# Kernel tuning notes

Hardware: AMD Instinct MI355X
Metric: run time of the kernel (lower is better)

Reference implementation:

```python
import jax, jax.numpy as jnp
import numpy as np

B = 4          # graphs
N = 8192       # coarse nodes (2048/graph)
M = 65536      # fine (skip) nodes (16384/graph)
E = 131072     # edges (32768/graph)
T = 16         # global tokens per graph
F_IN = 16      # dim of x and x_skip (concat -> in_channels = 32)
HID, OUT = 32, 16
ED, GD, EMB, H = 3, 1024, 64, 4
K = 3


def _make_pe(t, d):
    # PositionalEncoding buffer (sin/cos), deterministic constant
    position = np.arange(t, dtype=np.float32)[:, None]
    div = np.exp(np.arange(0, d, 2, dtype=np.float32) * (-np.log(10000.0) / d))
    pe = np.zeros((t, d), dtype=np.float32)
    pe[:, 0::2] = np.sin(position * div)
    pe[:, 1::2] = np.cos(position * div)
    return jnp.asarray(pe)


def setup_inputs():
    key = jax.random.key(0)
    ks = jax.random.split(key, 30)
    n, m, e = N // B, M // B, E // B
    inp = {}
    inp['x'] = jax.random.normal(ks[0], (N, F_IN), jnp.float32)
    inp['pos'] = jax.random.normal(ks[1], (N, 3), jnp.float32)
    inp['batch'] = jnp.repeat(jnp.arange(B), n)
    inp['x_skip'] = jax.random.normal(ks[2], (M, F_IN), jnp.float32)
    inp['pos_skip'] = jax.random.normal(ks[3], (M, 3), jnp.float32)
    inp['batch_skip'] = jnp.repeat(jnp.arange(B), m)
    off = jnp.repeat(jnp.arange(B) * m, e)
    inp['edge_index'] = jax.random.randint(ks[4], (2, E), 0, m) + off[None, :]
    inp['global_token'] = jax.random.normal(ks[5], (B * T, GD), jnp.float32)
    def lin(k, o, i, s):
        return jax.random.normal(k, (o, i), jnp.float32) * s
    inp['Wq_w'] = lin(ks[6], EMB, ED, 0.3); inp['Wq_b'] = jnp.zeros((EMB,), jnp.float32)
    inp['Wk_w'] = lin(ks[7], EMB, GD, 0.03); inp['Wk_b'] = jnp.zeros((EMB,), jnp.float32)
    inp['Wv_w'] = lin(ks[8], EMB, GD, 0.03); inp['Wv_b'] = jnp.zeros((EMB,), jnp.float32)
    inp['in_proj_w'] = lin(ks[9], 3 * EMB, EMB, 0.125); inp['in_proj_b'] = jnp.zeros((3 * EMB,), jnp.float32)
    inp['out_w'] = lin(ks[10], EMB, EMB, 0.125); inp['out_b'] = jnp.zeros((EMB,), jnp.float32)
    dims = [(2 * F_IN, HID), (HID, HID), (HID, OUT)]
    for i, (ci, co) in enumerate(dims):
        inp[f'nn_w{i}'] = lin(ks[11 + 3 * i], ci * co, ED + EMB, 0.05)
        inp[f'nn_b{i}'] = jnp.zeros((ci * co,), jnp.float32)
        inp[f'root{i}'] = jax.random.normal(ks[12 + 3 * i], (ci, co), jnp.float32) * (1.0 / np.sqrt(ci))
        inp[f'bias{i}'] = jnp.zeros((co,), jnp.float32)
    return inp


def reference(x, pos, batch, x_skip, pos_skip, batch_skip, edge_index, global_token,
              Wq_w, Wq_b, Wk_w, Wk_b, Wv_w, Wv_b, in_proj_w, in_proj_b, out_w, out_b,
              nn_w0, nn_b0, root0, bias0, nn_w1, nn_b1, root1, bias1, nn_w2, nn_b2, root2, bias2):
    # ---- knn_interpolate (k=3, inverse squared-distance weighting) ----
    # graphs are equal-sized by construction so per-graph knn == batched knn
    pos_b = pos.reshape(B, -1, 3)
    posk_b = pos_skip.reshape(B, -1, 3)
    d2 = ((posk_b ** 2).sum(-1)[:, :, None] + (pos_b ** 2).sum(-1)[:, None, :]
          - 2.0 * jnp.einsum('bmc,bnc->bmn', posk_b, pos_b))  # [B,m,n]
    neg, idx = jax.lax.top_k(-d2, K)                           # [B,m,K]
    w = 1.0 / jnp.maximum(-neg, 1e-16)
    x_b = x.reshape(B, -1, x.shape[-1])
    feats = jnp.take_along_axis(x_b[:, None, :, :], idx[:, :, :, None], axis=2)  # [B,m,K,F]
    xf = ((w[..., None] * feats).sum(2) / w.sum(2)[..., None]).reshape(M, -1)

    src, dst = edge_index[0], edge_index[1]
    pseudo = pos_skip[dst] - pos_skip[src]                     # patch_size is None
    edge_pos = (0.5 * (pos_skip[dst] + pos_skip[src])).reshape(B, -1, 3)
    gt = global_token.reshape(B, -1, global_token.shape[-1])
    pe = _make_pe(gt.shape[1], EMB)
    Q = edge_pos @ Wq_w.T + Wq_b                               # [B,Eb,EMB]
    Kt = gt @ Wk_w.T + Wk_b + pe                               # dropout in eval = identity
    Vt = gt @ Wv_w.T + Wv_b + pe
    # ---- MultiheadAttention (batch_first) ----
    wq, wk, wv = jnp.split(in_proj_w, 3, axis=0)
    bq, bk, bv = jnp.split(in_proj_b, 3, axis=0)
    hd = EMB // H
    def heads(t, w_, b_):
        t = t @ w_.T + b_
        return t.reshape(t.shape[0], t.shape[1], H, hd).transpose(0, 2, 1, 3)
    q, k_, v = heads(Q, wq, bq), heads(Kt, wk, bk), heads(Vt, wv, bv)
    att = jax.nn.softmax(jnp.einsum('bhqd,bhkd->bhqk', q, k_) / np.sqrt(hd).astype(np.float32), axis=-1)
    o = jnp.einsum('bhqk,bhkd->bhqd', att, v).transpose(0, 2, 1, 3).reshape(B, -1, EMB)
    o = o @ out_w.T + out_b
    pseudo = jnp.concatenate([pseudo, o.reshape(-1, EMB)], axis=-1)  # [E, 3+64]

    # ---- NNConv stack (gather -> edge MLP -> per-edge matmul -> scatter mean) ----
    h = jnp.concatenate([xf, x_skip], axis=1)                  # [M, 32]
    ones = jnp.ones((E,), jnp.float32)
    cnt = jnp.maximum(jax.ops.segment_sum(ones, dst, num_segments=M), 1.0)[:, None]
    for nw, nb, rt, bs in ((nn_w0, nn_b0, root0, bias0),
                           (nn_w1, nn_b1, root1, bias1),
                           (nn_w2, nn_b2, root2, bias2)):
        ci, co = rt.shape
        we = jax.nn.relu(pseudo @ nw.T + nb).reshape(E, ci, co)  # MLP (BN at default eval stats ~ identity)
        msg = jnp.einsum('ei,eio->eo', h[src], we)               # [E, co]
        aggr = jax.ops.segment_sum(msg, dst, num_segments=M) / cnt
        h = jax.nn.relu(aggr + h @ rt + bs)                      # drop_act=False -> relu every layer
    return h, pos_skip, batch_skip
```

## Files before the change

kernel.cpp:

```cpp
#include <hip/hip_runtime.h>
#include <math.h>

#define NB    4
#define NN    8192
#define MM    65536
#define EE    131072
#define NPG   2048

typedef short short8 __attribute__((ext_vector_type(8)));
typedef float f32x4  __attribute__((ext_vector_type(4)));

static __device__ inline unsigned short f2b(float f) {
    unsigned u = __float_as_uint(f);
    u += 0x7fffu + ((u >> 16) & 1u);
    return (unsigned short)(u >> 16);
}
static __device__ inline unsigned f2b_pack(float a, float b) {
    unsigned x = __float_as_uint(a); x += 0x7fffu + ((x >> 16) & 1u);
    unsigned y = __float_as_uint(b); y += 0x7fffu + ((y >> 16) & 1u);
    return (x >> 16) | (y & 0xffff0000u);
}
static __device__ inline short8 bc8(uint4 v) {
    union { uint4 u; short8 s; } c; c.u = v; return c.s;
}

__global__ __launch_bounds__(256)
void k_knn(const float* __restrict__ pos, const float* __restrict__ pos_skip,
           const float* __restrict__ x, const float* __restrict__ x_skip,
           const int* __restrict__ batch_skip,
           float* __restrict__ h0, float* __restrict__ out_pos,
           float* __restrict__ out_batch)
{
    __shared__ float4 cp[1024];
    __shared__ float  pk[8][32][3];
    __shared__ float  wFin[32][3];
    __shared__ int    iFin[32][3];

    int tid = threadIdx.x;
    int g = blockIdx.x >> 9;
    int cbase = g * NPG;
    int node = tid & 31;
    int slice = tid >> 5;
    int fbase = blockIdx.x * 32;
    int f = fbase + node;
    float fx = pos_skip[f * 3 + 0], fy = pos_skip[f * 3 + 1], fz = pos_skip[f * 3 + 2];

    float k0 = 3.4028235e38f, k1 = 3.4028235e38f, k2 = 3.4028235e38f;
#pragma unroll
    for (int p = 0; p < 2; ++p) {
        if (p) __syncthreads();
        for (int c = tid; c < 1024; c += 256) {
            int cc = cbase + p * 1024 + c;
            float px = pos[cc * 3 + 0];
            float py = pos[cc * 3 + 1];
            float pz = pos[cc * 3 + 2];
            cp[c] = make_float4(-2.f * px, -2.f * py, -2.f * pz,
                                px * px + py * py + pz * pz);
        }
        __syncthreads();
        const float4* cps = cp + slice * 128;
        unsigned ibase = (unsigned)(p * 128);
#pragma unroll 8
        for (int l = 0; l < 128; ++l) {
            float4 cc = cps[l];
            float d = fmaf(cc.x, fx, cc.w);
            d = fmaf(cc.y, fy, d);
            d = fmaf(cc.z, fz, d);
            float key = __uint_as_float((__float_as_uint(d) & 0xFFFFFF00u)
                                        | (ibase + (unsigned)l));
            float t = fmaxf(k1, key);
            k2 = fminf(k2, t);
            k1 = __builtin_amdgcn_fmed3f(k0, k1, key);
            k0 = fminf(k0, key);
        }
    }
    pk[slice][node][0] = k0; pk[slice][node][1] = k1; pk[slice][node][2] = k2;
    __syncthreads();

    if (tid < 32) {
        int n = tid;
        int fn = fbase + n;
        float gx = pos_skip[fn * 3 + 0], gy = pos_skip[fn * 3 + 1], gz = pos_skip[fn * 3 + 2];
        float gq = gx * gx + gy * gy + gz * gz;
        unsigned long long m0 = ~0ull, m1 = ~0ull, m2 = ~0ull;
#pragma unroll
        for (int s = 0; s < 8; ++s)
#pragma unroll
            for (int r = 0; r < 3; ++r) {
                unsigned key = __float_as_uint(pk[s][n][r]);
                unsigned pj = key & 255u;
                int c = cbase + (int)((pj >> 7) * 1024u + (unsigned)s * 128u + (pj & 127u));
                float px = pos[c * 3 + 0];
                float py = pos[c * 3 + 1];
                float pz = pos[c * 3 + 2];
                float d = gq + (px * px + py * py + pz * pz);
                d = fmaf(-2.f * px, gx, d);
                d = fmaf(-2.f * py, gy, d);
                d = fmaf(-2.f * pz, gz, d);
                d = fmaxf(d, 0.f);
                unsigned long long kk = ((unsigned long long)__float_as_uint(d) << 32) | (unsigned)c;
                unsigned long long t1 = m0 > kk ? m0 : kk; m0 = m0 < kk ? m0 : kk;
                unsigned long long t2 = m1 > t1 ? m1 : t1; m1 = m1 < t1 ? m1 : t1;
                m2 = m2 < t2 ? m2 : t2;
            }
        float d0 = __uint_as_float((unsigned)(m0 >> 32));
        float d1 = __uint_as_float((unsigned)(m1 >> 32));
        float d2 = __uint_as_float((unsigned)(m2 >> 32));
        float w0 = 1.f / fmaxf(d0, 1e-16f);
        float w1 = 1.f / fmaxf(d1, 1e-16f);
        float w2 = 1.f / fmaxf(d2, 1e-16f);
        float inv = 1.f / (w0 + w1 + w2);
        wFin[n][0] = w0 * inv; wFin[n][1] = w1 * inv; wFin[n][2] = w2 * inv;
        iFin[n][0] = (int)(m0 & 0xffffffffull);
        iFin[n][1] = (int)(m1 & 0xffffffffull);
        iFin[n][2] = (int)(m2 & 0xffffffffull);
        out_pos[fn * 3 + 0] = gx; out_pos[fn * 3 + 1] = gy; out_pos[fn * 3 + 2] = gz;
        out_batch[fn] = (float)batch_skip[fn];
    }
    __syncthreads();

    int n2 = tid >> 3, part = tid & 7;
    int f2 = fbase + n2;
    float4* h04 = (float4*)(h0 + (size_t)f2 * 32);
    if (part < 4) {
        const float4* x4 = (const float4*)x;
        float w0 = wFin[n2][0], w1 = wFin[n2][1], w2 = wFin[n2][2];
        int a0 = iFin[n2][0] * 4, a1 = iFin[n2][1] * 4, a2 = iFin[n2][2] * 4;
        float4 v0 = x4[a0 + part], v1 = x4[a1 + part], v2 = x4[a2 + part];
        float4 r;
        r.x = w0 * v0.x + w1 * v1.x + w2 * v2.x;
        r.y = w0 * v0.y + w1 * v1.y + w2 * v2.y;
        r.z = w0 * v0.z + w1 * v1.z + w2 * v2.z;
        r.w = w0 * v0.w + w1 * v1.w + w2 * v2.w;
        h04[part] = r;
    } else {
        const float4* xs4 = (const float4*)x_skip;
        h04[part] = xs4[f2 * 4 + (part - 4)];
    }
}

__global__ __launch_bounds__(128)
void k_tokens1(const float* __restrict__ gt,
               const float* __restrict__ Wk_w, const float* __restrict__ Wk_b,
               const float* __restrict__ Wv_w, const float* __restrict__ Wv_b,
               float* __restrict__ KtVt)
{
    int b = blockIdx.x >> 4;
    int t = blockIdx.x & 15;
    int which = threadIdx.x >> 6;
    int d = threadIdx.x & 63;
    const float* W = which ? Wv_w : Wk_w;
    const float* bias = which ? Wv_b : Wk_b;
    const float4* row = (const float4*)(gt + (size_t)(b * 16 + t) * 1024);
    const float4* wr = (const float4*)(W + (size_t)d * 1024);
    float acc = 0.f;
    for (int c = 0; c < 256; ++c) {
        float4 a = row[c], w = wr[c];
        acc += a.x * w.x; acc += a.y * w.y; acc += a.z * w.z; acc += a.w * w.w;
    }
    int i2 = d >> 1;
    float dv = expf((float)(2 * i2) * (-0.14391156831212787f));
    float ang = (float)t * dv;
    float pe = (d & 1) ? cosf(ang) : sinf(ang);
    KtVt[((size_t)(b * 2 + which) * 16 + t) * 64 + d] = acc + bias[d] + pe;
}

__global__ __launch_bounds__(256)
void k_tokens2(const float* __restrict__ KtVt,
               const float* __restrict__ in_proj_w, const float* __restrict__ in_proj_b,
               const float* __restrict__ out_w,
               const float* __restrict__ Wq_w, const float* __restrict__ Wq_b,
               float* __restrict__ Mfold, uint4* __restrict__ v2fG)
{
    int b = blockIdx.x;
    int tid = threadIdx.x;
    __shared__ float KtL[1024], VtL[1024], vv[1024], kproj[1024];
    __shared__ float v2L[4096];
    __shared__ float qWs[192], qbs[64];
    for (int idx = tid; idx < 1024; idx += 256) {
        KtL[idx] = KtVt[(size_t)(b * 2 + 0) * 1024 + idx];
        VtL[idx] = KtVt[(size_t)(b * 2 + 1) * 1024 + idx];
    }
    __syncthreads();
    for (int idx = tid; idx < 2048; idx += 256) {
        int which = idx >> 10; int td = idx & 1023; int t = td >> 6; int j = td & 63;
        int r = (which ? 128 : 64) + j;
        const float* w = in_proj_w + (size_t)r * 64;
        const float* src = which ? VtL : KtL;
        float acc = in_proj_b[r];
#pragma unroll 8
        for (int dd = 0; dd < 64; ++dd) acc += src[t * 64 + dd] * w[dd];
        if (which) vv[t * 64 + j] = acc;
        else kproj[t * 64 + j] = acc;
    }
    for (int idx = tid; idx < 192; idx += 256) {
        int c = idx >> 6; int j = idx & 63;
        float acc = 0.f;
        for (int dd = 0; dd < 64; ++dd) acc += in_proj_w[(size_t)j * 64 + dd] * Wq_w[dd * 3 + c];
        qWs[c * 64 + j] = acc;
    }
    for (int j = tid; j < 64; j += 256) {
        float acc = in_proj_b[j];
        for (int dd = 0; dd < 64; ++dd) acc += in_proj_w[(size_t)j * 64 + dd] * Wq_b[dd];
        qbs[j] = acc;
    }
    __syncthreads();
    for (int idx = tid; idx < 4096; idx += 256) {
        int jo = idx & 63; int th2 = idx >> 6; int h = th2 & 3; int t = th2 >> 2;
        float acc = 0.f;
#pragma unroll
        for (int dd = 0; dd < 16; ++dd)
            acc += vv[t * 64 + h * 16 + dd] * out_w[(size_t)jo * 64 + h * 16 + dd];
        v2L[(t * 4 + h) * 64 + jo] = acc;
    }
    {
        int th = tid >> 2, c = tid & 3;
        int t = th >> 2, h = th & 3;
        float acc = 0.f;
#pragma unroll
        for (int dd = h * 16; dd < h * 16 + 16; ++dd) {
            float w = (c == 0) ? qWs[dd] : (c == 1) ? qWs[64 + dd]
                    : (c == 2) ? qWs[128 + dd] : qbs[dd];
            acc += w * kproj[t * 64 + dd];
        }
        Mfold[((size_t)b * 64 + th) * 4 + c] = 0.25f * acc;
    }
    __syncthreads();
    for (int it = tid; it < 512; it += 256) {
        int lane = it & 63, fi = it >> 6;
        int mi = fi >> 1, step = fi & 1;
        int outd = mi * 16 + (lane & 15);
        int th0 = step * 32 + (lane >> 4) * 8;
        uint4 v;
        v.x = f2b_pack(v2L[(th0 + 0) * 64 + outd], v2L[(th0 + 1) * 64 + outd]);
        v.y = f2b_pack(v2L[(th0 + 2) * 64 + outd], v2L[(th0 + 3) * 64 + outd]);
        v.z = f2b_pack(v2L[(th0 + 4) * 64 + outd], v2L[(th0 + 5) * 64 + outd]);
        v.w = f2b_pack(v2L[(th0 + 6) * 64 + outd], v2L[(th0 + 7) * 64 + outd]);
        v2fG[((size_t)b * 8 + fi) * 64 + lane] = v;
    }
}

__global__ __launch_bounds__(256)
void k_edge_attn(const float* __restrict__ ps, const int* __restrict__ ei,
                 const float* __restrict__ Mfold, const uint4* __restrict__ v2f,
                 const float* __restrict__ ob,
                 unsigned short* __restrict__ Pf, float* __restrict__ cnt)
{
    __shared__ unsigned attL[4 * 64 * 34];
    int tid = threadIdx.x;
    int wave = tid >> 6, lane = tid & 63, q = lane >> 4, c15 = lane & 15;
    int g = blockIdx.x >> 7;
    int e = blockIdx.x * 256 + tid;
    int s = ei[e], d = ei[EE + e];
    atomicAdd(&cnt[d], 1.f);
    float sx = ps[s * 3], sy = ps[s * 3 + 1], sz = ps[s * 3 + 2];
    float dx = ps[d * 3], dy = ps[d * 3 + 1], dz = ps[d * 3 + 2];
    float px = dx - sx, py = dy - sy, pz = dz - sz;
    float ex = 0.5f * (dx + sx), ey = 0.5f * (dy + sy), ez = 0.5f * (dz + sz);

    const float4* Mg = (const float4*)Mfold + (size_t)g * 64;
    float sc[64];
#pragma unroll
    for (int th = 0; th < 64; ++th) {
        float4 m = Mg[th];
        sc[th] = ex * m.x + ey * m.y + ez * m.z + m.w;
    }
#pragma unroll
    for (int h = 0; h < 4; ++h) {
        float mx = sc[h];
#pragma unroll
        for (int t = 1; t < 16; ++t) mx = fmaxf(mx, sc[t * 4 + h]);
        float ssum = 0.f;
#pragma unroll
        for (int t = 0; t < 16; ++t) {
            float eo = expf(sc[t * 4 + h] - mx);
            sc[t * 4 + h] = eo; ssum += eo;
        }
        float inv = 1.f / ssum;
#pragma unroll
        for (int t = 0; t < 16; ++t) sc[t * 4 + h] *= inv;
    }
    unsigned* slab = attL + wave * 64 * 34;
#pragma unroll
    for (int k = 0; k < 16; ++k) {
        uint2 v;
        v.x = f2b_pack(sc[4 * k + 0], sc[4 * k + 1]);
        v.y = f2b_pack(sc[4 * k + 2], sc[4 * k + 3]);
        *(uint2*)&slab[lane * 34 + 2 * k] = v;
    }
    __syncthreads();

    uint4 v2a[4][2];
#pragma unroll
    for (int mi = 0; mi < 4; ++mi)
#pragma unroll
        for (int st = 0; st < 2; ++st)
            v2a[mi][st] = v2f[((size_t)g * 8 + mi * 2 + st) * 64 + lane];

    f32x4 acc[4][4];
#pragma unroll
    for (int mi = 0; mi < 4; ++mi)
#pragma unroll
        for (int nt = 0; nt < 4; ++nt) acc[mi][nt] = (f32x4){0.f, 0.f, 0.f, 0.f};

#pragma unroll
    for (int nt = 0; nt < 4; ++nt) {
        const unsigned* rb = &slab[(nt * 16 + c15) * 34];
        uint4 b0 = *(const uint4*)&rb[q * 4];
        uint4 b1 = *(const uint4*)&rb[16 + q * 4];
#pragma unroll
        for (int mi = 0; mi < 4; ++mi) {
            acc[mi][nt] = __builtin_amdgcn_mfma_f32_16x16x32_bf16(bc8(v2a[mi][0]), bc8(b0), acc[mi][nt], 0, 0, 0);
            acc[mi][nt] = __builtin_amdgcn_mfma_f32_16x16x32_bf16(bc8(v2a[mi][1]), bc8(b1), acc[mi][nt], 0, 0, 0);
        }
    }
    __syncthreads();

    float4 obv[4];
#pragma unroll
    for (int mi = 0; mi < 4; ++mi) obv[mi] = *(const float4*)(ob + mi * 16 + q * 4);
#pragma unroll
    for (int mi = 0; mi < 4; ++mi)
#pragma unroll
        for (int nt = 0; nt < 4; ++nt) {
            f32x4 a = acc[mi][nt];
            uint2 v;
            v.x = f2b_pack(a[0] + obv[mi].x, a[1] + obv[mi].y);
            v.y = f2b_pack(a[2] + obv[mi].z, a[3] + obv[mi].w);
            *(uint2*)&slab[(nt * 16 + c15) * 34 + mi * 8 + q * 2] = v;
        }
    __syncthreads();

    uint4* Pf4 = (uint4*)Pf;
#pragma unroll
    for (int et = 0; et < 4; ++et) {
        int etg = blockIdx.x * 16 + wave * 4 + et;
#pragma unroll
        for (int st = 0; st < 2; ++st) {
            uint4 w = *(const uint4*)&slab[(et * 16 + c15) * 34 + st * 16 + q * 4];
            Pf4[((size_t)etg * 3 + st) * 64 + lane] = w;
        }
    }
    int et2 = e >> 4, eL = e & 15;
    size_t tb = ((size_t)(et2 * 3 + 2) * 64 + 0 * 16 + eL) * 8;
    uint2 t0; t0.x = f2b_pack(px, py); t0.y = f2b_pack(pz, 1.0f);
    *(uint2*)(Pf + tb) = t0;
    uint2 z2; z2.x = 0u; z2.y = 0u;
    *(uint2*)(Pf + tb + 4) = z2;
#pragma unroll
    for (int quad = 1; quad < 4; ++quad) {
        size_t zb = ((size_t)(et2 * 3 + 2) * 64 + quad * 16 + eL) * 8;
        uint4 z4; z4.x = 0u; z4.y = 0u; z4.z = 0u; z4.w = 0u;
        *(uint4*)(Pf + zb) = z4;
    }
}

static __device__ inline void repack_one(const float* __restrict__ nw,
                                         const float* __restrict__ nb,
                                         unsigned short* __restrict__ Wf, int idx)
{
    int jj = idx & 7;
    int lane = (idx >> 3) & 63;
    int rest = idx >> 9;
    int s = rest % 3;
    int jt = rest / 3;
    int j = jt * 16 + (lane & 15);
    int k = s * 32 + (lane >> 4) * 8 + jj;
    float v;
    if (k < 64)       v = nw[(size_t)j * 67 + 3 + k];
    else if (k < 67)  v = nw[(size_t)j * 67 + (k - 64)];
    else if (k == 67) v = nb[j];
    else              v = 0.f;
    Wf[idx] = f2b(v);
}

__global__ __launch_bounds__(256)
void k_repackAll(const float* __restrict__ nw0, const float* __restrict__ nb0,
                 const float* __restrict__ nw1, const float* __restrict__ nb1,
                 const float* __restrict__ nw2, const float* __restrict__ nb2,
                 unsigned short* __restrict__ Wf0, unsigned short* __restrict__ Wf1,
                 unsigned short* __restrict__ Wf2)
{
    int idx = blockIdx.x * 256 + threadIdx.x;
    if (idx < 98304)        repack_one(nw0, nb0, Wf0, idx);
    else if (idx < 196608)  repack_one(nw1, nb1, Wf1, idx - 98304);
    else                    repack_one(nw2, nb2, Wf2, idx - 196608);
}

template<int CO>
__global__ __launch_bounds__(256, 4)
void k_conv_mfma(const uint4* __restrict__ Pf, const float* __restrict__ hin,
                 const int* __restrict__ ei, const uint4* __restrict__ Wf,
                 float* __restrict__ aggr)
{
    __shared__ float hL[128 * 36];
    __shared__ int sL[128];
    __shared__ int dL[128];
    constexpr int REDSZ = (CO == 16) ? 2 * 64 * 17 : 4;
    __shared__ float red[REDSZ];

    int tid = threadIdx.x;
    int e0 = blockIdx.x * 128;
    if (tid < 128) sL[tid] = ei[e0 + tid];
    else           dL[tid - 128] = ei[EE + e0 + (tid - 128)];
    __syncthreads();
    for (int idx = tid; idx < 1024; idx += 256) {
        int row = idx >> 3, c = idx & 7;
        const float4* hr = (const float4*)(hin + (size_t)sL[row] * 32);
        *(float4*)&hL[row * 36 + c * 4] = hr[c];
    }
    __syncthreads();

    int wave = tid >> 6, lane = tid & 63, quad = lane >> 4, col = lane & 15;
    int group = wave >> 1, half = wave & 1;

    uint4 a[4][3];
    int et0 = blockIdx.x * 8 + group * 4;
#pragma unroll
    for (int st = 0; st < 4; ++st)
#pragma unroll
        for (int s = 0; s < 3; ++s)
            a[st][s] = Pf[((size_t)(et0 + st) * 3 + s) * 64 + lane];

    float msg[4][4];
#pragma unroll
    for (int st = 0; st < 4; ++st)
#pragma unroll
        for (int r = 0; r < 4; ++r) msg[st][r] = 0.f;

    int ibase = (CO == 32) ? 0 : half * 16;
    constexpr int NI2 = (CO == 32) ? 16 : 8;

    for (int i2 = 0; i2 < NI2; ++i2) {
        float2 hv2[4][4];
#pragma unroll
        for (int st = 0; st < 4; ++st)
#pragma unroll
            for (int r = 0; r < 4; ++r)
                hv2[st][r] = *(const float2*)&hL[(group * 64 + st * 16 + quad * 4 + r) * 36
                                                 + ibase + i2 * 2];
#pragma unroll
        for (int ii = 0; ii < 2; ++ii) {
            int i = ibase + i2 * 2 + ii;
            int jt = (CO == 32) ? (i * 2 + half) : i;
            uint4 b0 = Wf[((size_t)jt * 3 + 0) * 64 + lane];
            uint4 b1 = Wf[((size_t)jt * 3 + 1) * 64 + lane];
            uint4 b2 = Wf[((size_t)jt * 3 + 2) * 64 + lane];
#pragma unroll
            for (int st = 0; st < 4; ++st) {
                f32x4 c = {0.f, 0.f, 0.f, 0.f};
                c = __builtin_amdgcn_mfma_f32_16x16x32_bf16(bc8(a[st][0]), bc8(b0), c, 0, 0, 0);
                c = __builtin_amdgcn_mfma_f32_16x16x32_bf16(bc8(a[st][1]), bc8(b1), c, 0, 0, 0);
                c = __builtin_amdgcn_mfma_f32_16x16x32_bf16(bc8(a[st][2]), bc8(b2), c, 0, 0, 0);
#pragma unroll
                for (int r = 0; r < 4; ++r) {
                    float hv = ii ? hv2[st][r].y : hv2[st][r].x;
                    msg[st][r] += hv * fmaxf(c[r], 0.f);
                }
            }
        }
    }

    if (CO == 32) {
#pragma unroll
        for (int st = 0; st < 4; ++st)
#pragma unroll
            for (int r = 0; r < 4; ++r) {
                int dv = dL[group * 64 + st * 16 + quad * 4 + r];
                atomicAdd(&aggr[(size_t)dv * 32 + half * 16 + col], msg[st][r]);
            }
    } else {
        if (half == 1) {
#pragma unroll
            for (int st = 0; st < 4; ++st)
#pragma unroll
                for (int r = 0; r < 4; ++r)
                    red[group * 64 * 17 + lane * 17 + st * 4 + r] = msg[st][r];
        }
        __syncthreads();
        if (half == 0) {
#pragma unroll
            for (int st = 0; st < 4; ++st)
#pragma unroll
                for (int r = 0; r < 4; ++r) {
                    float m = msg[st][r] + red[group * 64 * 17 + lane * 17 + st * 4 + r];
                    int dv = dL[group * 64 + st * 16 + quad * 4 + r];
                    atomicAdd(&aggr[(size_t)dv * 16 + col], m);
                }
        }
    }
}

template<int CO>
__global__ __launch_bounds__(256)
void k_update(float* __restrict__ aggr, const float* __restrict__ cnt,
              const float* __restrict__ hin, const float* __restrict__ root,
              const float* __restrict__ bias, float* __restrict__ hout)
{
    __shared__ float rL[32 * CO];
    __shared__ float bL[CO];
    int tid = threadIdx.x;
    for (int idx = tid; idx < 32 * CO; idx += 256) rL[idx] = root[idx];
    if (tid < CO) bL[tid] = bias[tid];
    __syncthreads();
    int gid = blockIdx.x * 256 + tid;
    int v = gid / CO;
    int o = gid % CO;
    float acc = aggr[gid] / fmaxf(cnt[v], 1.f) + bL[o];
    aggr[gid] = 0.f;
    const float* hr = hin + (size_t)v * 32;
#pragma unroll
    for (int i = 0; i < 32; ++i) acc += hr[i] * rL[i * CO + o];
    hout[gid] = fmaxf(acc, 0.f);
}

extern "C" void kernel_launch(void* const* d_in, const int* in_sizes, int n_in,
                              void* d_out, int out_size, void* d_ws, size_t ws_size,
                              hipStream_t stream)
{
    const float* x          = (const float*)d_in[0];
    const float* pos        = (const float*)d_in[1];
    const float* x_skip     = (const float*)d_in[3];
    const float* pos_skip   = (const float*)d_in[4];
    const int*   batch_skip = (const int*)  d_in[5];
    const int*   ei         = (const int*)  d_in[6];
    const float* gt         = (const float*)d_in[7];
    const float* Wq_w       = (const float*)d_in[8];
    const float* Wq_b       = (const float*)d_in[9];
    const float* Wk_w       = (const float*)d_in[10];
    const float* Wk_b       = (const float*)d_in[11];
    const float* Wv_w       = (const float*)d_in[12];
    const float* Wv_b       = (const float*)d_in[13];
    const float* in_proj_w  = (const float*)d_in[14];
    const float* in_proj_b  = (const float*)d_in[15];
    const float* out_w      = (const float*)d_in[16];
    const float* out_b      = (const float*)d_in[17];
    const float* nn_w0 = (const float*)d_in[18]; const float* nn_b0 = (const float*)d_in[19];
    const float* root0 = (const float*)d_in[20]; const float* bias0 = (const float*)d_in[21];
    const float* nn_w1 = (const float*)d_in[22]; const float* nn_b1 = (const float*)d_in[23];
    const float* root1 = (const float*)d_in[24]; const float* bias1 = (const float*)d_in[25];
    const float* nn_w2 = (const float*)d_in[26]; const float* nn_b2 = (const float*)d_in[27];
    const float* root2 = (const float*)d_in[28]; const float* bias2 = (const float*)d_in[29];

    char* wsb = (char*)d_ws;
    size_t off = 0;
    auto carve = [&](size_t bytes) { char* p = wsb + off; off += (bytes + 255) & ~(size_t)255; return p; };
    float* aggr = (float*)carve((size_t)MM * 32 * 4);
    float* cnt  = (float*)carve((size_t)MM * 4);
    float* hA   = (float*)carve((size_t)MM * 32 * 4);
    float* hB   = (float*)carve((size_t)MM * 32 * 4);
    unsigned short* Pf  = (unsigned short*)carve((size_t)EE * 96 * 2);
    unsigned short* Wf0 = (unsigned short*)carve((size_t)1024 * 96 * 2);
    unsigned short* Wf1 = (unsigned short*)carve((size_t)1024 * 96 * 2);
    unsigned short* Wf2 = (unsigned short*)carve((size_t)512 * 96 * 2);
    float* Mfold = (float*)carve((size_t)NB * 64 * 4 * 4);
    uint4* v2f   = (uint4*)carve((size_t)NB * 8 * 64 * 16);
    float* KtVt  = (float*)carve((size_t)NB * 2 * 16 * 64 * 4);

    float* h_final   = (float*)d_out;
    float* out_pos   = (float*)d_out + (size_t)MM * 16;
    float* out_batch = (float*)d_out + (size_t)MM * 19;

    hipMemsetAsync(aggr, 0, ((size_t)MM * 32 + MM) * sizeof(float), stream);

    k_tokens1<<<64, 128, 0, stream>>>(gt, Wk_w, Wk_b, Wv_w, Wv_b, KtVt);
    k_tokens2<<<NB, 256, 0, stream>>>(KtVt, in_proj_w, in_proj_b, out_w, Wq_w, Wq_b,
                                      Mfold, v2f);
    k_knn<<<MM / 32, 256, 0, stream>>>(pos, pos_skip, x, x_skip, batch_skip,
                                       hA, out_pos, out_batch);
    k_edge_attn<<<EE / 256, 256, 0, stream>>>(pos_skip, ei, Mfold, v2f, out_b,
                                              Pf, cnt);
    k_repackAll<<<960, 256, 0, stream>>>(nn_w0, nn_b0, nn_w1, nn_b1, nn_w2, nn_b2,
                                         Wf0, Wf1, Wf2);

    k_conv_mfma<32><<<EE / 128, 256, 0, stream>>>((const uint4*)Pf, hA, ei, (const uint4*)Wf0, aggr);
    k_update<32><<<(MM * 32) / 256, 256, 0, stream>>>(aggr, cnt, hA, root0, bias0, hB);
    k_conv_mfma<32><<<EE / 128, 256, 0, stream>>>((const uint4*)Pf, hB, ei, (const uint4*)Wf1, aggr);
    k_update<32><<<(MM * 32) / 256, 256, 0, stream>>>(aggr, cnt, hB, root1, bias1, hA);
    k_conv_mfma<16><<<EE / 128, 256, 0, stream>>>((const uint4*)Pf, hA, ei, (const uint4*)Wf2, aggr);
    k_update<16><<<(MM * 16) / 256, 256, 0, stream>>>(aggr, cnt, hA, root2, bias2, h_final);
}
```

Measured before the change: 366.2 us.

## Register-block kNN so each thread scans candidates for four fine nodes

The kNN kernel now handles 64 fine nodes per block instead of 32. Each thread keeps top-3 state for four fine nodes and scans a 64-candidate slice, so every LDS candidate load is reused across four distance evaluations. Coarse positions are staged into shared memory half as often per fine node, and the block count is halved. The cost is more registers per thread, a 16-way merge in the final stage instead of 8-way, and a longer serial refine step running on only 64 threads.

```diff
diff --git a/kernel.cpp b/kernel.cpp
--- a/kernel.cpp
+++ b/kernel.cpp
@@ -32,20 +32,28 @@
            float* __restrict__ out_batch)
 {
     __shared__ float4 cp[1024];
-    __shared__ float  pk[8][32][3];
-    __shared__ float  wFin[32][3];
-    __shared__ int    iFin[32][3];
+    __shared__ float  pk[16][64][3];
+    __shared__ float  wFin[64][3];
+    __shared__ int    iFin[64][3];
 
     int tid = threadIdx.x;
-    int g = blockIdx.x >> 9;
+    int g = blockIdx.x >> 8;
     int cbase = g * NPG;
-    int node = tid & 31;
-    int slice = tid >> 5;
-    int fbase = blockIdx.x * 32;
-    int f = fbase + node;
-    float fx = pos_skip[f * 3 + 0], fy = pos_skip[f * 3 + 1], fz = pos_skip[f * 3 + 2];
-
-    float k0 = 3.4028235e38f, k1 = 3.4028235e38f, k2 = 3.4028235e38f;
+    int slice = tid & 15;
+    int grp = tid >> 4;
+    int fbase = blockIdx.x * 64;
+
+    float fx[4], fy[4], fz[4];
+    float k0[4], k1[4], k2[4];
+#pragma unroll
+    for (int j = 0; j < 4; ++j) {
+        int f = fbase + grp * 4 + j;
+        fx[j] = pos_skip[f * 3 + 0];
+        fy[j] = pos_skip[f * 3 + 1];
+        fz[j] = pos_skip[f * 3 + 2];
+        k0[j] = 3.4028235e38f; k1[j] = 3.4028235e38f; k2[j] = 3.4028235e38f;
+    }
+
 #pragma unroll
     for (int p = 0; p < 2; ++p) {
         if (p) __syncthreads();
@@ -58,38 +66,45 @@
                                 px * px + py * py + pz * pz);
         }
         __syncthreads();
-        const float4* cps = cp + slice * 128;
-        unsigned ibase = (unsigned)(p * 128);
-#pragma unroll 8
-        for (int l = 0; l < 128; ++l) {
+        const float4* cps = cp + slice * 64;
+        unsigned ibase = (unsigned)(p * 64);
+#pragma unroll 4
+        for (int l = 0; l < 64; ++l) {
             float4 cc = cps[l];
-            float d = fmaf(cc.x, fx, cc.w);
-            d = fmaf(cc.y, fy, d);
-            d = fmaf(cc.z, fz, d);
-            float key = __uint_as_float((__float_as_uint(d) & 0xFFFFFF00u)
-                                        | (ibase + (unsigned)l));
-            float t = fmaxf(k1, key);
-            k2 = fminf(k2, t);
-            k1 = __builtin_amdgcn_fmed3f(k0, k1, key);
-            k0 = fminf(k0, key);
-        }
-    }
-    pk[slice][node][0] = k0; pk[slice][node][1] = k1; pk[slice][node][2] = k2;
-    __syncthreads();
-
-    if (tid < 32) {
+            unsigned idx = ibase + (unsigned)l;
+#pragma unroll
+            for (int j = 0; j < 4; ++j) {
+                float d = fmaf(cc.x, fx[j], cc.w);
+                d = fmaf(cc.y, fy[j], d);
+                d = fmaf(cc.z, fz[j], d);
+                float key = __uint_as_float((__float_as_uint(d) & 0xFFFFFF00u) | idx);
+                float t = fmaxf(k1[j], key);
+                k2[j] = fminf(k2[j], t);
+                k1[j] = __builtin_amdgcn_fmed3f(k0[j], k1[j], key);
+                k0[j] = fminf(k0[j], key);
+            }
+        }
+    }
+#pragma unroll
+    for (int j = 0; j < 4; ++j) {
+        int n = grp * 4 + j;
+        pk[slice][n][0] = k0[j]; pk[slice][n][1] = k1[j]; pk[slice][n][2] = k2[j];
+    }
+    __syncthreads();
+
+    if (tid < 64) {
         int n = tid;
         int fn = fbase + n;
         float gx = pos_skip[fn * 3 + 0], gy = pos_skip[fn * 3 + 1], gz = pos_skip[fn * 3 + 2];
         float gq = gx * gx + gy * gy + gz * gz;
         unsigned long long m0 = ~0ull, m1 = ~0ull, m2 = ~0ull;
 #pragma unroll
-        for (int s = 0; s < 8; ++s)
+        for (int s = 0; s < 16; ++s)
 #pragma unroll
             for (int r = 0; r < 3; ++r) {
                 unsigned key = __float_as_uint(pk[s][n][r]);
                 unsigned pj = key & 255u;
-                int c = cbase + (int)((pj >> 7) * 1024u + (unsigned)s * 128u + (pj & 127u));
+                int c = cbase + (int)((pj >> 6) * 1024u + (unsigned)s * 64u + (pj & 63u));
                 float px = pos[c * 3 + 0];
                 float py = pos[c * 3 + 1];
                 float pz = pos[c * 3 + 2];
@@ -119,23 +134,31 @@
     }
     __syncthreads();
 
-    int n2 = tid >> 3, part = tid & 7;
+    int n2 = tid >> 2, part = tid & 3;
     int f2 = fbase + n2;
     float4* h04 = (float4*)(h0 + (size_t)f2 * 32);
-    if (part < 4) {
+    if (part < 2) {
         const float4* x4 = (const float4*)x;
         float w0 = wFin[n2][0], w1 = wFin[n2][1], w2 = wFin[n2][2];
         int a0 = iFin[n2][0] * 4, a1 = iFin[n2][1] * 4, a2 = iFin[n2][2] * 4;
-        float4 v0 = x4[a0 + part], v1 = x4[a1 + part], v2 = x4[a2 + part];
-        float4 r;
-        r.x = w0 * v0.x + w1 * v1.x + w2 * v2.x;
-        r.y = w0 * v0.y + w1 * v1.y + w2 * v2.y;
-        r.z = w0 * v0.z + w1 * v1.z + w2 * v2.z;
-        r.w = w0 * v0.w + w1 * v1.w + w2 * v2.w;
-        h04[part] = r;
+#pragma unroll
+        for (int j = 0; j < 2; ++j) {
+            int cj = part * 2 + j;
+            float4 v0 = x4[a0 + cj], v1 = x4[a1 + cj], v2 = x4[a2 + cj];
+            float4 r;
+            r.x = w0 * v0.x + w1 * v1.x + w2 * v2.x;
+            r.y = w0 * v0.y + w1 * v1.y + w2 * v2.y;
+            r.z = w0 * v0.z + w1 * v1.z + w2 * v2.z;
+            r.w = w0 * v0.w + w1 * v1.w + w2 * v2.w;
+            h04[cj] = r;
+        }
     } else {
         const float4* xs4 = (const float4*)x_skip;
-        h04[part] = xs4[f2 * 4 + (part - 4)];
+#pragma unroll
+        for (int j = 0; j < 2; ++j) {
+            int cj = (part - 2) * 2 + j;
+            h04[4 + cj] = xs4[f2 * 4 + cj];
+        }
     }
 }
 
@@ -566,7 +589,7 @@
     k_tokens1<<<64, 128, 0, stream>>>(gt, Wk_w, Wk_b, Wv_w, Wv_b, KtVt);
     k_tokens2<<<NB, 256, 0, stream>>>(KtVt, in_proj_w, in_proj_b, out_w, Wq_w, Wq_b,
                                       Mfold, v2f);
-    k_knn<<<MM / 32, 256, 0, stream>>>(pos, pos_skip, x, x_skip, batch_skip,
+    k_knn<<<MM / 64, 256, 0, stream>>>(pos, pos_skip, x, x_skip, batch_skip,
                                        hA, out_pos, out_batch);
     k_edge_attn<<<EE / 256, 256, 0, stream>>>(pos_skip, ei, Mfold, v2f, out_b,
                                               Pf, cnt);
```

Result: slower. 393.8 us (+7.6%).
